# Performance work log

Measured on AMD Instinct MI355X. Metric: run time of the kernel, lower is better.

The kernel has to match this reference:

```python
import jax, jax.numpy as jnp
import numpy as np
from jax import lax

N_SPINS = 32   # num_spins
HILDIM = 2     # hilbert space dim
HID = 512      # hidden_size
NLAYERS = 3    # num_layers
NSAMP = 2048   # numsamples (acts as the RNN time axis, per torch's unbatched semantics)


def setup_inputs() -> dict:
    key = jax.random.key(0)
    ks = jax.random.split(key, 11)
    k = 1.0 / np.sqrt(HID)  # torch.nn.RNN default init bound
    u = lambda kk, shape: jax.random.uniform(kk, shape, jnp.float32, -k, k)
    return {
        "samples": jax.random.randint(ks[0], (NSAMP, N_SPINS), 0, HILDIM),
        "Wih0": u(ks[1], (N_SPINS, HID, HILDIM)),        # layer-0 input weights per spin
        "Whh0": u(ks[2], (N_SPINS, HID, HID)),
        "bih0": u(ks[3], (N_SPINS, HID)),
        "bhh0": u(ks[4], (N_SPINS, HID)),
        "Wih": u(ks[5], (N_SPINS, NLAYERS - 1, HID, HID)),  # layers 1..L-1 per spin
        "Whh": u(ks[6], (N_SPINS, NLAYERS - 1, HID, HID)),
        "bih": u(ks[7], (N_SPINS, NLAYERS - 1, HID)),
        "bhh": u(ks[8], (N_SPINS, NLAYERS - 1, HID)),
        "Wd": u(ks[9], (N_SPINS, 2, HID)),                  # dense head per spin
        "bd": u(ks[10], (N_SPINS, 2)),
    }


def _rnn_scan(x_seq, h0, Wi, Wh, bi, bh):
    # Faithful torch.nn.RNN (tanh) over the sample axis (torch treats the 2D
    # [numsamples, feat] input as an unbatched sequence of length numsamples).
    def step(h, x):
        h = jnp.tanh(x @ Wi.T + bi + h @ Wh.T + bh)
        return h, h
    hT, ys = lax.scan(step, h0, x_seq)
    return ys, hT  # ys: [S, H], hT: [H]


def reference(samples, Wih0, Whh0, bih0, bhh0, Wih, Whh, bih, bhh, Wd, bd):
    # Implements RNN.probability(samples)
    S, N = samples.shape
    H = Whh0.shape[-1]
    hd = Wih0.shape[-1]
    L = Wih.shape[1] + 1
    onehot = jax.nn.one_hot(samples, hd, dtype=jnp.float32)          # [S, N, hd]
    # inputs fed to spin i: zeros for i=0, one_hot(samples[:, i-1]) after
    xs = jnp.concatenate([jnp.zeros((1, S, hd), jnp.float32),
                          jnp.transpose(onehot, (1, 0, 2))[:-1]], axis=0)  # [N, S, hd]

    def spin_step(state, per):
        # state: [L, H] hidden carried across spins (as in the torch code)
        x, Wi0, Wh0, bi0, bh0, WiL, WhL, biL, bhL, Wdi, bdi = per
        new_state = []
        y, hT = _rnn_scan(x, state[0], Wi0, Wh0, bi0, bh0)
        new_state.append(hT)
        for l in range(WiL.shape[0]):  # small static loop over layers 1..L-1
            y, hT = _rnn_scan(y, state[l + 1], WiL[l], WhL[l], biL[l], bhL[l])
            new_state.append(hT)
        p = jax.nn.softmax(y @ Wdi.T + bdi, axis=-1)  # [S, 2]
        return jnp.stack(new_state), p

    state0 = jnp.zeros((L, H), jnp.float32)
    _, probs = lax.scan(
        spin_step, state0,
        (xs, Wih0, Whh0, bih0, bhh0, Wih, Whh, bih, bhh, Wd, bd))
    probs = jnp.transpose(probs, (1, 0, 2))                          # [S, N, 2]
    return jnp.prod(jnp.sum(probs * onehot, axis=2), axis=1)         # [S]
```

## Files before the change

### kernel.cpp

```cpp
#include <hip/hip_runtime.h>
#include <stdint.h>

typedef unsigned long long u64;

#define SPS   2048
#define NSPIN 32
#define H     512
#define NSTEP (SPS*NSPIN)
#define TPB   512
#define ROWS  64
#define CHK   8
#define KT    64
#define NL    3

__device__ __forceinline__ u64 ld_agent(const u64* p){
  return __hip_atomic_load(p, __ATOMIC_RELAXED, __HIP_MEMORY_SCOPE_AGENT);
}
__device__ __forceinline__ void st_agent(u64* p, u64 v){
  __hip_atomic_store(p, v, __ATOMIC_RELAXED, __HIP_MEMORY_SCOPE_AGENT);
}
__device__ __forceinline__ unsigned ldu_agent(const unsigned* p){
  return __hip_atomic_load(p, __ATOMIC_RELAXED, __HIP_MEMORY_SCOPE_AGENT);
}
__device__ __forceinline__ void stu_agent(unsigned* p, unsigned v){
  __hip_atomic_store(p, v, __ATOMIC_RELAXED, __HIP_MEMORY_SCOPE_AGENT);
}

__device__ __forceinline__ float poll_pkt(const u64* p, unsigned tag){
  u64 v = ld_agent(p);
  int guard = 0;
  while ((unsigned)(v >> 32) != tag){
    __builtin_amdgcn_s_sleep(1);
    v = ld_agent(p);
    if (++guard > (1<<22)) break;
  }
  return __uint_as_float((unsigned)(v & 0xffffffffu));
}

__global__ void init_prog(unsigned* prog){
  prog[threadIdx.x] = 0;
}

__global__ __launch_bounds__(TPB)
void rnn_pipeline(const int* __restrict__ samples,
                  const float* __restrict__ Wih0, const float* __restrict__ Whh0,
                  const float* __restrict__ bih0, const float* __restrict__ bhh0,
                  const float* __restrict__ Wih,  const float* __restrict__ Whh,
                  const float* __restrict__ bih,  const float* __restrict__ bhh,
                  const float* __restrict__ Wd,   const float* __restrict__ bd,
                  float* __restrict__ out,
                  u64* __restrict__ ring, unsigned* __restrict__ prog,
                  int depth)
{
  const int bid = blockIdx.x;
  const int tid = threadIdx.x;
  const int dmask = depth - 1;

  __shared__ float lds_h[2][H];
  __shared__ float lds_y[2][H];
  __shared__ float lds_part[2][CHK][ROWS];
  __shared__ float lds_acc[SPS];
  __shared__ float lds_red[2][2][8];

  if (bid == 24){
    for (int t = tid; t < SPS; t += TPB) lds_acc[t] = 1.0f;
    __syncthreads();
    u64* ring2 = ring + (size_t)2*depth*H;
    const int w = tid >> 6, lane = tid & 63;
    float wd0=0.f, wd1=0.f, b0=0.f, b1=0.f;
    for (int u = 0; u < NSTEP; ++u){
      const int i = u >> 11, t = u & (SPS-1), par = u & 1;
      if ((u & (SPS-1)) == 0){
        wd0 = Wd[((size_t)i*2+0)*H + tid];
        wd1 = Wd[((size_t)i*2+1)*H + tid];
        b0 = bd[i*2+0]; b1 = bd[i*2+1];
      }
      float y = poll_pkt(&ring2[(size_t)(u & dmask)*H + tid], (unsigned)(u+1));
      float p0 = wd0*y, p1 = wd1*y;
      #pragma unroll
      for (int o = 32; o > 0; o >>= 1){
        p0 += __shfl_down(p0, o);
        p1 += __shfl_down(p1, o);
      }
      if (lane == 0){ lds_red[par][0][w] = p0; lds_red[par][1][w] = p1; }
      __syncthreads();
      if (tid == 0){
        float z0 = b0, z1 = b1;
        #pragma unroll
        for (int q = 0; q < 8; ++q){ z0 += lds_red[par][0][q]; z1 += lds_red[par][1][q]; }
        const int sel = samples[t*NSPIN + i];
        const float m  = fmaxf(z0, z1);
        const float e0 = expf(z0 - m), e1 = expf(z1 - m);
        lds_acc[t] *= (sel ? e1 : e0) / (e0 + e1);
      }
      if (((u & 63) == 63) && tid == 0) stu_agent(&prog[bid*16], (unsigned)(u+1));
    }
    if (tid == 0) stu_agent(&prog[bid*16], (unsigned)NSTEP);
    __syncthreads();
    for (int t = tid; t < SPS; t += TPB) out[t] = lds_acc[t];
    return;
  }

  const int layer = bid >> 3, g = bid & 7;
  const int c = tid >> 6, r = tid & 63;
  const int row = g*ROWS + r;
  u64* ringL  = ring + (size_t)layer*depth*H;
  u64* ringIn = ring + (size_t)(layer > 0 ? layer-1 : 0)*depth*H;
  const bool has_wi = (layer > 0);

  float wh[KT], wi[KT];
  float bsum = 0.f, w0c = 0.f, w1c = 0.f;

  for (int u = 0; u < NSTEP; ++u){
    const int i = u >> 11, t = u & (SPS-1), par = u & 1;

    if ((u & (SPS-1)) == 0){
      const float* whp = (layer == 0)
        ? Whh0 + ((size_t)i*H + row)*H + c*KT
        : Whh  + (((size_t)i*(NL-1) + (layer-1))*H + row)*H + c*KT;
      #pragma unroll
      for (int j = 0; j < KT; j += 4){
        float4 v4 = *(const float4*)(whp + j);
        wh[j] = v4.x; wh[j+1] = v4.y; wh[j+2] = v4.z; wh[j+3] = v4.w;
      }
      if (has_wi){
        const float* wip = Wih + (((size_t)i*(NL-1) + (layer-1))*H + row)*H + c*KT;
        #pragma unroll
        for (int j = 0; j < KT; j += 4){
          float4 v4 = *(const float4*)(wip + j);
          wi[j] = v4.x; wi[j+1] = v4.y; wi[j+2] = v4.z; wi[j+3] = v4.w;
        }
      }
      if (c == 0){
        if (layer == 0){
          bsum = bih0[i*H + row] + bhh0[i*H + row];
          w0c  = Wih0[((size_t)i*H + row)*2 + 0];
          w1c  = Wih0[((size_t)i*H + row)*2 + 1];
        } else {
          bsum = bih[((size_t)i*(NL-1) + (layer-1))*H + row]
               + bhh[((size_t)i*(NL-1) + (layer-1))*H + row];
        }
      }
    }

    if (((u & 63) == 0) && (u + 64 > depth) && tid == 0){
      const unsigned need = (unsigned)(u + 64 - depth);
      const int cfirst = (layer < 2) ? (layer+1)*8 : 24;
      const int ccount = (layer < 2) ? 8 : 1;
      int guard = 0;
      for (;;){
        unsigned mn = 0xffffffffu;
        for (int q = 0; q < ccount; ++q){
          unsigned pv = ldu_agent(&prog[(cfirst+q)*16]);
          mn = (pv < mn) ? pv : mn;
        }
        if (mn >= need) break;
        __builtin_amdgcn_s_sleep(8);
        if (++guard > (1<<20)) break;
      }
    }

    if (u > 0)
      lds_h[par][tid] = poll_pkt(&ringL[(size_t)((u-1) & dmask)*H + tid], (unsigned)u);
    else
      lds_h[par][tid] = 0.0f;
    if (has_wi)
      lds_y[par][tid] = poll_pkt(&ringIn[(size_t)(u & dmask)*H + tid], (unsigned)(u+1));
    __syncthreads();

    const float* hs = &lds_h[par][c*KT];
    float a0=0.f, a1=0.f, a2=0.f, a3=0.f;
    if (has_wi){
      const float* ys = &lds_y[par][c*KT];
      #pragma unroll
      for (int j = 0; j < KT; j += 4){
        a0 = fmaf(wh[j+0], hs[j+0], a0); a1 = fmaf(wh[j+1], hs[j+1], a1);
        a2 = fmaf(wh[j+2], hs[j+2], a2); a3 = fmaf(wh[j+3], hs[j+3], a3);
        a0 = fmaf(wi[j+0], ys[j+0], a0); a1 = fmaf(wi[j+1], ys[j+1], a1);
        a2 = fmaf(wi[j+2], ys[j+2], a2); a3 = fmaf(wi[j+3], ys[j+3], a3);
      }
    } else {
      #pragma unroll
      for (int j = 0; j < KT; j += 4){
        a0 = fmaf(wh[j+0], hs[j+0], a0); a1 = fmaf(wh[j+1], hs[j+1], a1);
        a2 = fmaf(wh[j+2], hs[j+2], a2); a3 = fmaf(wh[j+3], hs[j+3], a3);
      }
    }
    lds_part[par][c][r] = (a0 + a1) + (a2 + a3);
    __syncthreads();

    if (c == 0){
      float s = 0.f;
      #pragma unroll
      for (int q = 0; q < CHK; ++q) s += lds_part[par][q][r];
      float add = bsum;
      if (layer == 0 && i > 0){
        const int bit = samples[t*NSPIN + (i-1)];
        add += bit ? w1c : w0c;
      }
      const float hv = tanhf(s + add);
      st_agent(&ringL[(size_t)(u & dmask)*H + row],
               ((u64)(unsigned)(u+1) << 32) | (u64)__float_as_uint(hv));
    }
    if (((u & 63) == 63) && tid == 0) stu_agent(&prog[bid*16], (unsigned)(u+1));
  }
  if (tid == 0) stu_agent(&prog[bid*16], (unsigned)NSTEP);
}

extern "C" void kernel_launch(void* const* d_in, const int* in_sizes, int n_in,
                              void* d_out, int out_size, void* d_ws, size_t ws_size,
                              hipStream_t stream)
{
  const int*   samples = (const int*)  d_in[0];
  const float* Wih0    = (const float*)d_in[1];
  const float* Whh0    = (const float*)d_in[2];
  const float* bih0    = (const float*)d_in[3];
  const float* bhh0    = (const float*)d_in[4];
  const float* Wih     = (const float*)d_in[5];
  const float* Whh     = (const float*)d_in[6];
  const float* bih     = (const float*)d_in[7];
  const float* bhh     = (const float*)d_in[8];
  const float* Wd      = (const float*)d_in[9];
  const float* bd      = (const float*)d_in[10];

  int depth = 256;
  while (depth > 2 && (size_t)3*depth*H*sizeof(u64) + 4096 > ws_size) depth >>= 1;

  u64*      ring = (u64*)d_ws;
  unsigned* prog = (unsigned*)((char*)d_ws + (size_t)3*depth*H*sizeof(u64));

  init_prog<<<1, 512, 0, stream>>>(prog);
  rnn_pipeline<<<25, TPB, 0, stream>>>(samples, Wih0, Whh0, bih0, bhh0,
                                       Wih, Whh, bih, bhh, Wd, bd,
                                       (float*)d_out, ring, prog, depth);
}
```

Baseline: 115.5 ms.

## Precompute input projection off critical path and use wave-shuffle row reduction

Each recurrent block now computes the input-weight product for the next step after publishing its hidden state, so only the hidden-state product sits on the serial dependency chain. The K reduction is remapped so 8 lanes within a wave share a row and finish with shuffles, which removes one barrier and the shared-memory partial-sum buffer per step. Upstream activations are prefetched two steps ahead into a triple buffer, and sample bits are staged in LDS. Polling spins briefly before sleeping. The risks are tighter ring-depth margins and more register pressure.

New measurement: 290.7 ms. +151.8%, slower.

```diff
diff --git a/kernel.cpp b/kernel.cpp
--- a/kernel.cpp
+++ b/kernel.cpp
@@ -8,9 +8,6 @@
 #define H     512
 #define NSTEP (SPS*NSPIN)
 #define TPB   512
-#define ROWS  64
-#define CHK   8
-#define KT    64
 #define NL    3
 
 __device__ __forceinline__ u64 ld_agent(const u64* p){
@@ -28,18 +25,16 @@
 
 __device__ __forceinline__ float poll_pkt(const u64* p, unsigned tag){
   u64 v = ld_agent(p);
-  int guard = 0;
+  int n = 0;
   while ((unsigned)(v >> 32) != tag){
-    __builtin_amdgcn_s_sleep(1);
+    if (++n > 8) __builtin_amdgcn_s_sleep(1);
     v = ld_agent(p);
-    if (++guard > (1<<22)) break;
-  }
-  return __uint_as_float((unsigned)(v & 0xffffffffu));
-}
-
-__global__ void init_prog(unsigned* prog){
-  prog[threadIdx.x] = 0;
-}
+    if (n > (1<<21)) break;
+  }
+  return __uint_as_float((unsigned)v);
+}
+
+__global__ void init_prog(unsigned* prog){ prog[threadIdx.x] = 0; }
 
 __global__ __launch_bounds__(TPB)
 void rnn_pipeline(const int* __restrict__ samples,
@@ -56,26 +51,29 @@
   const int tid = threadIdx.x;
   const int dmask = depth - 1;
 
-  __shared__ float lds_h[2][H];
-  __shared__ float lds_y[2][H];
-  __shared__ float lds_part[2][CHK][ROWS];
+  __shared__ __align__(16) float lds_h[2][H];
+  __shared__ __align__(16) float lds_y[3][H];
+  __shared__ int   lds_bits[SPS];
   __shared__ float lds_acc[SPS];
   __shared__ float lds_red[2][2][8];
 
   if (bid == 24){
-    for (int t = tid; t < SPS; t += TPB) lds_acc[t] = 1.0f;
-    __syncthreads();
+    for (int tt = tid; tt < SPS; tt += TPB) lds_acc[tt] = 1.0f;
     u64* ring2 = ring + (size_t)2*depth*H;
     const int w = tid >> 6, lane = tid & 63;
     float wd0=0.f, wd1=0.f, b0=0.f, b1=0.f;
+    __syncthreads();
     for (int u = 0; u < NSTEP; ++u){
       const int i = u >> 11, t = u & (SPS-1), par = u & 1;
       if ((u & (SPS-1)) == 0){
+        __syncthreads();
+        for (int tt = tid; tt < SPS; tt += TPB)
+          lds_bits[tt] = samples[tt*NSPIN + i];
         wd0 = Wd[((size_t)i*2+0)*H + tid];
         wd1 = Wd[((size_t)i*2+1)*H + tid];
         b0 = bd[i*2+0]; b1 = bd[i*2+1];
       }
-      float y = poll_pkt(&ring2[(size_t)(u & dmask)*H + tid], (unsigned)(u+1));
+      const float y = poll_pkt(&ring2[(size_t)(u & dmask)*H + tid], (unsigned)(u+1));
       float p0 = wd0*y, p1 = wd1*y;
       #pragma unroll
       for (int o = 32; o > 0; o >>= 1){
@@ -83,67 +81,119 @@
         p1 += __shfl_down(p1, o);
       }
       if (lane == 0){ lds_red[par][0][w] = p0; lds_red[par][1][w] = p1; }
+      if (tid == 510 && (u & 31) == 31) stu_agent(&prog[24*16], (unsigned)(u+1));
       __syncthreads();
       if (tid == 0){
         float z0 = b0, z1 = b1;
         #pragma unroll
         for (int q = 0; q < 8; ++q){ z0 += lds_red[par][0][q]; z1 += lds_red[par][1][q]; }
-        const int sel = samples[t*NSPIN + i];
         const float m  = fmaxf(z0, z1);
         const float e0 = expf(z0 - m), e1 = expf(z1 - m);
-        lds_acc[t] *= (sel ? e1 : e0) / (e0 + e1);
-      }
-      if (((u & 63) == 63) && tid == 0) stu_agent(&prog[bid*16], (unsigned)(u+1));
-    }
-    if (tid == 0) stu_agent(&prog[bid*16], (unsigned)NSTEP);
-    __syncthreads();
-    for (int t = tid; t < SPS; t += TPB) out[t] = lds_acc[t];
+        lds_acc[t] *= (lds_bits[t] ? e1 : e0) / (e0 + e1);
+      }
+    }
+    if (tid == 510) stu_agent(&prog[24*16], (unsigned)NSTEP);
+    __syncthreads();
+    for (int tt = tid; tt < SPS; tt += TPB) out[tt] = lds_acc[tt];
     return;
   }
 
   const int layer = bid >> 3, g = bid & 7;
-  const int c = tid >> 6, r = tid & 63;
-  const int row = g*ROWS + r;
+  const int w = tid >> 6, l = tid & 63;
+  const int kc   = l & 7;
+  const int rsub = l >> 3;
+  const int row  = g*64 + 8*w + rsub;
+  const bool leader = (kc == 0);
+  const bool has_y  = (layer > 0);
   u64* ringL  = ring + (size_t)layer*depth*H;
   u64* ringIn = ring + (size_t)(layer > 0 ? layer-1 : 0)*depth*H;
-  const bool has_wi = (layer > 0);
-
-  float wh[KT], wi[KT];
-  float bsum = 0.f, w0c = 0.f, w1c = 0.f;
+
+  float wh[64], wi[64];
+  float bsum = 0.f, w0c = 0.f, w1c = 0.f, py = 0.f;
+
+  if (has_y){
+    lds_y[0][tid] = poll_pkt(&ringIn[(size_t)(0 & dmask)*H + tid], 1u);
+    lds_y[1][tid] = poll_pkt(&ringIn[(size_t)(1 & dmask)*H + tid], 2u);
+    __syncthreads();
+  }
 
   for (int u = 0; u < NSTEP; ++u){
-    const int i = u >> 11, t = u & (SPS-1), par = u & 1;
+    const int i = u >> 11, t = u & (SPS-1), hb = u & 1;
 
     if ((u & (SPS-1)) == 0){
+      __syncthreads();
+      if (layer == 0 && i > 0){
+        for (int tt = tid; tt < SPS; tt += TPB)
+          lds_bits[tt] = samples[tt*NSPIN + (i-1)];
+      }
       const float* whp = (layer == 0)
-        ? Whh0 + ((size_t)i*H + row)*H + c*KT
-        : Whh  + (((size_t)i*(NL-1) + (layer-1))*H + row)*H + c*KT;
+        ? Whh0 + ((size_t)i*H + row)*H
+        : Whh  + (((size_t)i*(NL-1) + (layer-1))*H + row)*H;
       #pragma unroll
-      for (int j = 0; j < KT; j += 4){
-        float4 v4 = *(const float4*)(whp + j);
-        wh[j] = v4.x; wh[j+1] = v4.y; wh[j+2] = v4.z; wh[j+3] = v4.w;
-      }
-      if (has_wi){
-        const float* wip = Wih + (((size_t)i*(NL-1) + (layer-1))*H + row)*H + c*KT;
+      for (int jj = 0; jj < 16; ++jj){
+        const int j = (jj + kc) & 15;
+        const float4 v = *(const float4*)(whp + kc*64 + 4*j);
+        wh[4*jj+0]=v.x; wh[4*jj+1]=v.y; wh[4*jj+2]=v.z; wh[4*jj+3]=v.w;
+      }
+      if (has_y){
+        const float* wip = Wih + (((size_t)i*(NL-1) + (layer-1))*H + row)*H;
         #pragma unroll
-        for (int j = 0; j < KT; j += 4){
-          float4 v4 = *(const float4*)(wip + j);
-          wi[j] = v4.x; wi[j+1] = v4.y; wi[j+2] = v4.z; wi[j+3] = v4.w;
-        }
-      }
-      if (c == 0){
+        for (int jj = 0; jj < 16; ++jj){
+          const int j = (jj + kc) & 15;
+          const float4 v = *(const float4*)(wip + kc*64 + 4*j);
+          wi[4*jj+0]=v.x; wi[4*jj+1]=v.y; wi[4*jj+2]=v.z; wi[4*jj+3]=v.w;
+        }
+      }
+      if (leader){
         if (layer == 0){
           bsum = bih0[i*H + row] + bhh0[i*H + row];
           w0c  = Wih0[((size_t)i*H + row)*2 + 0];
           w1c  = Wih0[((size_t)i*H + row)*2 + 1];
         } else {
-          bsum = bih[((size_t)i*(NL-1) + (layer-1))*H + row]
-               + bhh[((size_t)i*(NL-1) + (layer-1))*H + row];
-        }
-      }
-    }
-
-    if (((u & 63) == 0) && (u + 64 > depth) && tid == 0){
+          bsum = bih[((size_t)i*(NL-1)+(layer-1))*H + row]
+               + bhh[((size_t)i*(NL-1)+(layer-1))*H + row];
+        }
+      }
+      if (has_y){
+        const float* ysrc = &lds_y[u % 3][kc*64];
+        float c0=0.f,c1=0.f,c2=0.f,c3=0.f;
+        #pragma unroll
+        for (int jj = 0; jj < 16; ++jj){
+          const int j = (jj + kc) & 15;
+          const float4 yv = *(const float4*)(ysrc + 4*j);
+          c0 = fmaf(wi[4*jj+0], yv.x, c0); c1 = fmaf(wi[4*jj+1], yv.y, c1);
+          c2 = fmaf(wi[4*jj+2], yv.z, c2); c3 = fmaf(wi[4*jj+3], yv.w, c3);
+        }
+        py = (c0+c1)+(c2+c3);
+      }
+    }
+
+    {
+      const u64* ph = &ringL[(size_t)((u-1) & dmask)*H + tid];
+      const u64* pq = &ringIn[(size_t)((u+2) & dmask)*H + tid];
+      const bool needh = (u > 0);
+      const bool needy = has_y && (u+2) < NSTEP;
+      const unsigned tagh = (unsigned)u, tagy = (unsigned)(u+3);
+      u64 vh = needh ? ld_agent(ph) : 0;
+      u64 vy = needy ? ld_agent(pq) : 0;
+      bool okh = !needh, oky = !needy;
+      float rh = 0.f, ry = 0.f;
+      int n = 0;
+      for (;;){
+        if (!okh && (unsigned)(vh >> 32) == tagh){ okh = true; rh = __uint_as_float((unsigned)vh); }
+        if (!oky && (unsigned)(vy >> 32) == tagy){ oky = true; ry = __uint_as_float((unsigned)vy); }
+        if (okh && oky) break;
+        if (++n > 8) __builtin_amdgcn_s_sleep(1);
+        if (!okh) vh = ld_agent(ph);
+        if (!oky) vy = ld_agent(pq);
+        if (n > (1<<21)) break;
+      }
+      lds_h[hb][tid] = rh;
+      if (needy) lds_y[(u+2) % 3][tid] = ry;
+    }
+
+    if (tid == 510 && (u & 31) == 31) stu_agent(&prog[bid*16], (unsigned)(u+1));
+    if (tid == 509 && (u & 63) == 0 && (u + 64) > depth){
       const unsigned need = (unsigned)(u + 64 - depth);
       const int cfirst = (layer < 2) ? (layer+1)*8 : 24;
       const int ccount = (layer < 2) ? 8 : 1;
@@ -151,8 +201,8 @@
       for (;;){
         unsigned mn = 0xffffffffu;
         for (int q = 0; q < ccount; ++q){
-          unsigned pv = ldu_agent(&prog[(cfirst+q)*16]);
-          mn = (pv < mn) ? pv : mn;
+          const unsigned pv = ldu_agent(&prog[(cfirst+q)*16]);
+          mn = pv < mn ? pv : mn;
         }
         if (mn >= need) break;
         __builtin_amdgcn_s_sleep(8);
@@ -160,51 +210,43 @@
       }
     }
 
-    if (u > 0)
-      lds_h[par][tid] = poll_pkt(&ringL[(size_t)((u-1) & dmask)*H + tid], (unsigned)u);
-    else
-      lds_h[par][tid] = 0.0f;
-    if (has_wi)
-      lds_y[par][tid] = poll_pkt(&ringIn[(size_t)(u & dmask)*H + tid], (unsigned)(u+1));
-    __syncthreads();
-
-    const float* hs = &lds_h[par][c*KT];
-    float a0=0.f, a1=0.f, a2=0.f, a3=0.f;
-    if (has_wi){
-      const float* ys = &lds_y[par][c*KT];
-      #pragma unroll
-      for (int j = 0; j < KT; j += 4){
-        a0 = fmaf(wh[j+0], hs[j+0], a0); a1 = fmaf(wh[j+1], hs[j+1], a1);
-        a2 = fmaf(wh[j+2], hs[j+2], a2); a3 = fmaf(wh[j+3], hs[j+3], a3);
-        a0 = fmaf(wi[j+0], ys[j+0], a0); a1 = fmaf(wi[j+1], ys[j+1], a1);
-        a2 = fmaf(wi[j+2], ys[j+2], a2); a3 = fmaf(wi[j+3], ys[j+3], a3);
-      }
-    } else {
-      #pragma unroll
-      for (int j = 0; j < KT; j += 4){
-        a0 = fmaf(wh[j+0], hs[j+0], a0); a1 = fmaf(wh[j+1], hs[j+1], a1);
-        a2 = fmaf(wh[j+2], hs[j+2], a2); a3 = fmaf(wh[j+3], hs[j+3], a3);
-      }
-    }
-    lds_part[par][c][r] = (a0 + a1) + (a2 + a3);
-    __syncthreads();
-
-    if (c == 0){
-      float s = 0.f;
-      #pragma unroll
-      for (int q = 0; q < CHK; ++q) s += lds_part[par][q][r];
-      float add = bsum;
-      if (layer == 0 && i > 0){
-        const int bit = samples[t*NSPIN + (i-1)];
-        add += bit ? w1c : w0c;
-      }
-      const float hv = tanhf(s + add);
+    __syncthreads();
+
+    float a0 = py, a1 = 0.f, a2 = 0.f, a3 = 0.f;
+    const float* hsrc = &lds_h[hb][kc*64];
+    #pragma unroll
+    for (int jj = 0; jj < 16; ++jj){
+      const int j = (jj + kc) & 15;
+      const float4 hv = *(const float4*)(hsrc + 4*j);
+      a0 = fmaf(wh[4*jj+0], hv.x, a0); a1 = fmaf(wh[4*jj+1], hv.y, a1);
+      a2 = fmaf(wh[4*jj+2], hv.z, a2); a3 = fmaf(wh[4*jj+3], hv.w, a3);
+    }
+    float p = (a0 + a1) + (a2 + a3);
+    p += __shfl_down(p, 4);
+    p += __shfl_down(p, 2);
+    p += __shfl_down(p, 1);
+    if (leader){
+      float s = p + bsum;
+      if (layer == 0 && i > 0) s += lds_bits[t] ? w1c : w0c;
+      const float hv = tanhf(s);
       st_agent(&ringL[(size_t)(u & dmask)*H + row],
                ((u64)(unsigned)(u+1) << 32) | (u64)__float_as_uint(hv));
     }
-    if (((u & 63) == 63) && tid == 0) stu_agent(&prog[bid*16], (unsigned)(u+1));
-  }
-  if (tid == 0) stu_agent(&prog[bid*16], (unsigned)NSTEP);
+
+    if (has_y && ((u+1) & (SPS-1)) != 0 && (u+1) < NSTEP){
+      const float* ysrc = &lds_y[(u+1) % 3][kc*64];
+      float c0=0.f,c1=0.f,c2=0.f,c3=0.f;
+      #pragma unroll
+      for (int jj = 0; jj < 16; ++jj){
+        const int j = (jj + kc) & 15;
+        const float4 yv = *(const float4*)(ysrc + 4*j);
+        c0 = fmaf(wi[4*jj+0], yv.x, c0); c1 = fmaf(wi[4*jj+1], yv.y, c1);
+        c2 = fmaf(wi[4*jj+2], yv.z, c2); c3 = fmaf(wi[4*jj+3], yv.w, c3);
+      }
+      py = (c0+c1)+(c2+c3);
+    }
+  }
+  if (tid == 510) stu_agent(&prog[bid*16], (unsigned)NSTEP);
 }
 
 extern "C" void kernel_launch(void* const* d_in, const int* in_sizes, int n_in,
```
